# Kernel optimization log

Measured on AMD Instinct MI355X. Metric: run time of the kernel, lower is better.

## Reference

```python
import jax, jax.numpy as jnp
import numpy as np

B, C_IN, H, W = 4, 3, 512, 512
KH = KW = 3
K = KH * KW
C_OUT = 3
HO, WO = H - 2, W - 2  # valid conv, stride 1, no padding


def setup_inputs() -> dict:
    key = jax.random.key(0)
    k1, k2, k3, k4, k5, k6 = jax.random.split(key, 6)
    x = jax.random.normal(k1, (B, C_IN, H, W), dtype=jnp.float32)
    # conv1: Conv2d(3, 18, 3) -> predicts offsets (2*kh*kw = 18 channels)
    w1 = jax.random.normal(k2, (18, C_IN, KH, KW), dtype=jnp.float32) * 0.05
    b1 = jax.random.normal(k3, (18,), dtype=jnp.float32) * 0.05
    # conv2: DeformConv2d(3, 3, 3) weight + bias
    w2 = jax.random.normal(k4, (C_OUT, C_IN, KH, KW), dtype=jnp.float32) * 0.1
    b2 = jax.random.normal(k5, (C_OUT,), dtype=jnp.float32) * 0.1
    return {"x": x, "w1": w1, "b1": b1, "w2": w2, "b2": b2}


def _bilinear_gather(img, y, x):
    # img: [B, C, H, W]; y, x: [B, K, Ho, Wo] float sampling coords.
    # Bilinear interpolation with zeros outside the image (torchvision semantics).
    y0 = jnp.floor(y)
    x0 = jnp.floor(x)
    dy = y - y0
    dx = x - x0
    out = jnp.zeros((img.shape[0], img.shape[1]) + y.shape[1:], dtype=img.dtype)
    for iy, wy in ((y0, 1.0 - dy), (y0 + 1.0, dy)):
        for ix, wx in ((x0, 1.0 - dx), (x0 + 1.0, dx)):
            valid = (iy >= 0) & (iy < H) & (ix >= 0) & (ix < W)
            yi = jnp.clip(iy, 0, H - 1).astype(jnp.int32)
            xi = jnp.clip(ix, 0, W - 1).astype(jnp.int32)
            w = jnp.where(valid, wy * wx, 0.0)  # [B,K,Ho,Wo]
            g = jax.vmap(lambda im, a, b: im[:, a, b])(img, yi, xi)  # [B,C,K,Ho,Wo]
            out = out + g * w[:, None]
    return out


def _forward(x, w1, b1, w2, b2):
    dn = ("NCHW", "OIHW", "NCHW")
    # offset-predicting conv: [B, 18, Ho, Wo]
    offs = jax.lax.conv_general_dilated(x, w1, (1, 1), "VALID", dimension_numbers=dn)
    offs = offs + b1[None, :, None, None]
    # torchvision layout: channel 2k = dy, 2k+1 = dx for kernel tap k (row-major)
    off = offs.reshape(B, K, 2, HO, WO)
    ky = jnp.repeat(jnp.arange(KH, dtype=jnp.float32), KW)  # [K]
    kx = jnp.tile(jnp.arange(KW, dtype=jnp.float32), KH)    # [K]
    gy = jnp.arange(HO, dtype=jnp.float32)[None, None, :, None]
    gx = jnp.arange(WO, dtype=jnp.float32)[None, None, None, :]
    sy = gy + ky[None, :, None, None] + off[:, :, 0]  # [B,K,Ho,Wo]
    sx = gx + kx[None, :, None, None] + off[:, :, 1]
    val = _bilinear_gather(x, sy, sx)  # [B,C,K,Ho,Wo]
    w2r = w2.reshape(C_OUT, C_IN, K)
    out = jnp.einsum("ock,bckij->boij", w2r, val) + b2[None, :, None, None]
    return out


def reference(x, w1, b1, w2, b2):
    return _forward(x, w1, b1, w2, b2)
```

## Files before the change

### kernel.cpp

```cpp
#include <hip/hip_runtime.h>

#define BB 4
#define CIN 3
#define HH 512
#define WW 512
#define KK 9
#define COUT 3
#define HO 510
#define WO 510
#define HW (HH * WW)
#define HOWO (HO * WO)

#define PR 518
#define PC 520
#define PADR 3
#define PADC 4
#define XP_BYTES ((size_t)BB * PR * PC * sizeof(uint2))

typedef __fp16 h2 __attribute__((ext_vector_type(2)));

__device__ __forceinline__ h2 pkrtz(float a, float b) {
    return __builtin_amdgcn_cvt_pkrtz(a, b);
}
__device__ __forceinline__ float fdot2f(h2 a, h2 b, float c) {
    return __builtin_amdgcn_fdot2(a, b, c, false);
}
__device__ __forceinline__ h2 uint_as_h2(unsigned u) {
    return __builtin_bit_cast(h2, u);
}
__device__ __forceinline__ unsigned h2_as_uint(h2 h) {
    return __builtin_bit_cast(unsigned, h);
}
__device__ __forceinline__ float w1e(const float* w1, int ch, int c, int r, int s) {
    return w1[ch * 27 + c * 9 + r * 3 + s];
}

__global__ __launch_bounds__(256) void repack_padh(
    const float* __restrict__ x, uint2* __restrict__ xp)
{
    const int idx = blockIdx.x * blockDim.x + threadIdx.x;
    const int total = BB * PR * PC;
    if (idx >= total) return;
    const int b = idx / (PR * PC);
    const int rem = idx - b * (PR * PC);
    const int y = rem / PC;
    const int xc = rem - y * PC;
    const int ys = y - PADR;
    const int xs = xc - PADC;
    uint2 v = make_uint2(0u, 0u);
    if ((unsigned)ys < (unsigned)HH && (unsigned)xs < (unsigned)WW) {
        const float* xb = x + (size_t)b * CIN * HW;
        const int p = ys * WW + xs;
        v.x = h2_as_uint(pkrtz(xb[p], xb[HW + p]));
        v.y = h2_as_uint(pkrtz(xb[2 * HW + p], 0.f));
    }
    xp[idx] = v;
}

__global__ __launch_bounds__(256) void deform_fused5(
    const uint2* __restrict__ xp,
    const float* __restrict__ w1,
    const float* __restrict__ b1,
    const float* __restrict__ w2,
    const float* __restrict__ b2,
    float* __restrict__ out)
{
    __shared__ uint4 s_w1h[KK * 9];
    __shared__ float s_b[18];
    __shared__ float s_w2[KK * 12];
    __shared__ float s_b2[COUT];

    if (threadIdx.x < KK * 9) {
        const int k = threadIdx.x / 9;
        const int pos = threadIdx.x % 9;
        const int r = pos / 3, s = pos % 3;
        uint4 u;
        u.x = h2_as_uint(pkrtz(w1e(w1, 2 * k, 0, r, s), w1e(w1, 2 * k, 1, r, s)));
        u.y = h2_as_uint(pkrtz(w1e(w1, 2 * k, 2, r, s), 0.f));
        u.z = h2_as_uint(pkrtz(w1e(w1, 2 * k + 1, 0, r, s), w1e(w1, 2 * k + 1, 1, r, s)));
        u.w = h2_as_uint(pkrtz(w1e(w1, 2 * k + 1, 2, r, s), 0.f));
        s_w1h[threadIdx.x] = u;
    }
    for (int t = threadIdx.x; t < KK * 12; t += 256) {
        const int k = t / 12;
        const int q = t % 12;
        s_w2[t] = (q < 9) ? w2[(q / 3) * 27 + (q % 3) * 9 + k] : 0.f;
    }
    if (threadIdx.x < 18) s_b[threadIdx.x] = b1[threadIdx.x];
    if (threadIdx.x < COUT) s_b2[threadIdx.x] = b2[threadIdx.x];
    __syncthreads();

    constexpr int WP = WO / 2;
    const int idx = blockIdx.x * 256 + threadIdx.x;
    if (idx >= BB * HO * WP) return;
    const int jp = idx % WP;
    const int t1 = idx / WP;
    const int i = t1 % HO;
    const int b = t1 / HO;
    const int j = jp * 2;

    const uint2* xb2 = xp + (size_t)b * (PR * PC);

    h2 p01[3][4], p2p[3][4];
#pragma unroll
    for (int r = 0; r < 3; ++r) {
        const int base = (i + r + PADR) * PC + (j + PADC);
        const uint4 qa = *reinterpret_cast<const uint4*>(xb2 + base);
        const uint4 qb = *reinterpret_cast<const uint4*>(xb2 + base + 2);
        p01[r][0] = uint_as_h2(qa.x); p2p[r][0] = uint_as_h2(qa.y);
        p01[r][1] = uint_as_h2(qa.z); p2p[r][1] = uint_as_h2(qa.w);
        p01[r][2] = uint_as_h2(qb.x); p2p[r][2] = uint_as_h2(qb.y);
        p01[r][3] = uint_as_h2(qb.z); p2p[r][3] = uint_as_h2(qb.w);
    }

    unsigned pk0[KK], pk1[KK];
#pragma unroll
    for (int k = 0; k < KK; ++k) {
        float dy0 = s_b[2 * k], dx0 = s_b[2 * k + 1];
        float dy1 = dy0, dx1 = dx0;
        const uint4* wk = &s_w1h[k * 9];
#pragma unroll
        for (int r = 0; r < 3; ++r)
#pragma unroll
            for (int s = 0; s < 3; ++s) {
                const uint4 wq = wk[r * 3 + s];
                const h2 wy01 = uint_as_h2(wq.x);
                const h2 wy2x = uint_as_h2(wq.y);
                const h2 wx01 = uint_as_h2(wq.z);
                const h2 wx2x = uint_as_h2(wq.w);
                dy0 = fdot2f(wy01, p01[r][s], dy0);
                dy0 = fdot2f(wy2x, p2p[r][s], dy0);
                dx0 = fdot2f(wx01, p01[r][s], dx0);
                dx0 = fdot2f(wx2x, p2p[r][s], dx0);
                dy1 = fdot2f(wy01, p01[r][s + 1], dy1);
                dy1 = fdot2f(wy2x, p2p[r][s + 1], dy1);
                dx1 = fdot2f(wx01, p01[r][s + 1], dx1);
                dx1 = fdot2f(wx2x, p2p[r][s + 1], dx1);
            }
        pk0[k] = h2_as_uint(pkrtz(dy0, dx0));
        pk1[k] = h2_as_uint(pkrtz(dy1, dx1));
    }

    const float fi = (float)(i + PADR);
    const float fj = (float)(j + PADC);
    float acc00 = s_b2[0], acc01 = s_b2[1], acc02 = s_b2[2];
    float acc10 = s_b2[0], acc11 = s_b2[1], acc12 = s_b2[2];

#pragma unroll
    for (int k = 0; k < KK; ++k) {
        const float4* wk4 = reinterpret_cast<const float4*>(&s_w2[k * 12]);
        const float4 a = wk4[0];
        const float4 bbv = wk4[1];
        const float cw = s_w2[k * 12 + 8];
        const float ry = fi + (float)(k / 3);
        const float rx = fj + (float)(k % 3);

#pragma unroll
        for (int p = 0; p < 2; ++p) {
            const h2 d = uint_as_h2(p ? pk1[k] : pk0[k]);
            const float syp = ry + (float)d.x;
            const float sxp = rx + (float)p + (float)d.y;
            const int y0 = (int)syp;
            const int x0 = (int)sxp;
            const float fy = syp - (float)y0;
            const float fx = sxp - (float)x0;

            const int a00 = y0 * PC + x0;
            const uint2 c00 = xb2[a00];
            const uint2 c01 = xb2[a00 + 1];
            const uint2 c10 = xb2[a00 + PC];
            const uint2 c11 = xb2[a00 + PC + 1];

            const float wy0 = 1.f - fy, wx0 = 1.f - fx;
            const float w00 = wy0 * wx0, w01 = wy0 * fx;
            const float w10 = fy * wx0, w11 = fy * fx;

            const h2 g00 = uint_as_h2(c00.x), e00 = uint_as_h2(c00.y);
            const h2 g01 = uint_as_h2(c01.x), e01 = uint_as_h2(c01.y);
            const h2 g10 = uint_as_h2(c10.x), e10 = uint_as_h2(c10.y);
            const h2 g11 = uint_as_h2(c11.x), e11 = uint_as_h2(c11.y);

            const float v0 = w00 * (float)g00.x + w01 * (float)g01.x +
                             w10 * (float)g10.x + w11 * (float)g11.x;
            const float v1 = w00 * (float)g00.y + w01 * (float)g01.y +
                             w10 * (float)g10.y + w11 * (float)g11.y;
            const float v2 = w00 * (float)e00.x + w01 * (float)e01.x +
                             w10 * (float)e10.x + w11 * (float)e11.x;

            const float r0 = a.x * v0 + a.y * v1 + a.z * v2;
            const float r1 = a.w * v0 + bbv.x * v1 + bbv.y * v2;
            const float r2 = bbv.z * v0 + bbv.w * v1 + cw * v2;
            if (p == 0) {
                acc00 += r0; acc01 += r1; acc02 += r2;
            } else {
                acc10 += r0; acc11 += r1; acc12 += r2;
            }
        }
    }

    float* ob = out + (size_t)b * COUT * HOWO + (size_t)i * WO + j;
    {
        float2 st;
        st.x = acc00; st.y = acc10;
        *reinterpret_cast<float2*>(&ob[0 * HOWO]) = st;
        st.x = acc01; st.y = acc11;
        *reinterpret_cast<float2*>(&ob[1 * HOWO]) = st;
        st.x = acc02; st.y = acc12;
        *reinterpret_cast<float2*>(&ob[2 * HOWO]) = st;
    }
}

__global__ __launch_bounds__(256) void deform_fused_kernel(
    const float* __restrict__ x, const float* __restrict__ w1,
    const float* __restrict__ b1, const float* __restrict__ w2,
    const float* __restrict__ b2, float* __restrict__ out)
{
    __shared__ float s_w1[18 * 27];
    __shared__ float s_b1[18];
    __shared__ float s_w2[COUT * CIN * KK];
    __shared__ float s_b2[COUT];
    for (int t = threadIdx.x; t < 18 * 27; t += blockDim.x) s_w1[t] = w1[t];
    if (threadIdx.x < 18) s_b1[threadIdx.x] = b1[threadIdx.x];
    if (threadIdx.x < COUT * CIN * KK) s_w2[threadIdx.x] = w2[threadIdx.x];
    if (threadIdx.x < COUT) s_b2[threadIdx.x] = b2[threadIdx.x];
    __syncthreads();
    const int idx = blockIdx.x * blockDim.x + threadIdx.x;
    if (idx >= BB * HOWO) return;
    const int j = idx % WO;
    const int tmp = idx / WO;
    const int i = tmp % HO;
    const int b = tmp / HO;
    const float* xb = x + (size_t)b * CIN * HW;
    float patch[CIN][3][3];
#pragma unroll
    for (int c = 0; c < CIN; ++c)
#pragma unroll
        for (int r = 0; r < 3; ++r)
#pragma unroll
            for (int s = 0; s < 3; ++s)
                patch[c][r][s] = xb[c * HW + (i + r) * WW + (j + s)];
    float acc0 = s_b2[0], acc1 = s_b2[1], acc2 = s_b2[2];
#pragma unroll
    for (int k = 0; k < KK; ++k) {
        const int ky = k / 3, kx = k % 3;
        float dy = s_b1[2 * k], dx = s_b1[2 * k + 1];
        const float* wy = &s_w1[(2 * k) * 27];
        const float* wx = &s_w1[(2 * k + 1) * 27];
        int t = 0;
#pragma unroll
        for (int c = 0; c < CIN; ++c)
#pragma unroll
            for (int r = 0; r < 3; ++r)
#pragma unroll
                for (int s = 0; s < 3; ++s, ++t) {
                    const float pv = patch[c][r][s];
                    dy += pv * wy[t];
                    dx += pv * wx[t];
                }
        const float sy = (float)(i + ky) + dy;
        const float sx = (float)(j + kx) + dx;
        const float y0f = floorf(sy), x0f = floorf(sx);
        const float fy = sy - y0f, fx = sx - x0f;
        const int y0 = (int)y0f, x0 = (int)x0f;
        float v0 = 0.f, v1 = 0.f, v2 = 0.f;
#pragma unroll
        for (int cy = 0; cy < 2; ++cy) {
            const int iy = y0 + cy;
            const float wyf = cy ? fy : (1.f - fy);
            const bool vy = (iy >= 0) && (iy < HH);
            const int iyc = iy < 0 ? 0 : (iy > HH - 1 ? HH - 1 : iy);
#pragma unroll
            for (int cx = 0; cx < 2; ++cx) {
                const int ix = x0 + cx;
                const float wxf = cx ? fx : (1.f - fx);
                const bool vx = (ix >= 0) && (ix < WW);
                const int ixc = ix < 0 ? 0 : (ix > WW - 1 ? WW - 1 : ix);
                const float wgt = (vy && vx) ? (wyf * wxf) : 0.f;
                const int off = iyc * WW + ixc;
                v0 += wgt * xb[0 * HW + off];
                v1 += wgt * xb[1 * HW + off];
                v2 += wgt * xb[2 * HW + off];
            }
        }
#pragma unroll
        for (int o = 0; o < COUT; ++o) {
            const float c0 = s_w2[(o * CIN + 0) * KK + k];
            const float c1 = s_w2[(o * CIN + 1) * KK + k];
            const float c2 = s_w2[(o * CIN + 2) * KK + k];
            const float contrib = c0 * v0 + c1 * v1 + c2 * v2;
            if (o == 0) acc0 += contrib;
            else if (o == 1) acc1 += contrib;
            else acc2 += contrib;
        }
    }
    float* ob = out + (size_t)b * COUT * HOWO + (size_t)i * WO + j;
    ob[0 * HOWO] = acc0;
    ob[1 * HOWO] = acc1;
    ob[2 * HOWO] = acc2;
}

extern "C" void kernel_launch(void* const* d_in, const int* in_sizes, int n_in,
                              void* d_out, int out_size, void* d_ws, size_t ws_size,
                              hipStream_t stream) {
    const float* x  = (const float*)d_in[0];
    const float* w1 = (const float*)d_in[1];
    const float* b1 = (const float*)d_in[2];
    const float* w2 = (const float*)d_in[3];
    const float* b2 = (const float*)d_in[4];
    float* out = (float*)d_out;

    if (ws_size >= XP_BYTES) {
        uint2* xp = (uint2*)d_ws;
        {
            const int total = BB * PR * PC;
            repack_padh<<<(total + 255) / 256, 256, 0, stream>>>(x, xp);
        }
        {
            const int total = BB * HO * (WO / 2);
            deform_fused5<<<(total + 255) / 256, 256, 0, stream>>>(
                xp, w1, b1, w2, b2, out);
        }
    } else {
        const int total = BB * HOWO;
        deform_fused_kernel<<<(total + 255) / 256, 256, 0, stream>>>(
            x, w1, b1, w2, b2, out);
    }
}
```

Baseline: 44.08 us.

## Pack horizontal pixel pairs in the repacked image and do bilinear blending in packed fp16

The repack kernel now stores each padded pixel together with its right neighbour as one 16-byte fp16 record. Each bilinear tap then needs two vector loads (top and bottom rows) instead of four 8-byte loads. The interpolation is done with packed half multiply-adds, and the output-channel mix uses fdot2 with fp16-packed w2 weights, which cuts scalar FMA and conversion work. The trade-offs are a workspace twice as large, roughly double the repack write traffic, and lower precision from accumulating the interpolation in fp16.

```diff
diff --git a/kernel.cpp b/kernel.cpp
--- a/kernel.cpp
+++ b/kernel.cpp
@@ -15,7 +15,7 @@
 #define PC 520
 #define PADR 3
 #define PADC 4
-#define XP_BYTES ((size_t)BB * PR * PC * sizeof(uint2))
+#define XP_BYTES ((size_t)BB * PR * PC * sizeof(uint4))
 
 typedef __fp16 h2 __attribute__((ext_vector_type(2)));
 
@@ -35,8 +35,8 @@
     return w1[ch * 27 + c * 9 + r * 3 + s];
 }
 
-__global__ __launch_bounds__(256) void repack_padh(
-    const float* __restrict__ x, uint2* __restrict__ xp)
+__global__ __launch_bounds__(256) void repack_pairh(
+    const float* __restrict__ x, uint4* __restrict__ xp)
 {
     const int idx = blockIdx.x * blockDim.x + threadIdx.x;
     const int total = BB * PR * PC;
@@ -46,19 +46,28 @@
     const int y = rem / PC;
     const int xc = rem - y * PC;
     const int ys = y - PADR;
-    const int xs = xc - PADC;
-    uint2 v = make_uint2(0u, 0u);
-    if ((unsigned)ys < (unsigned)HH && (unsigned)xs < (unsigned)WW) {
-        const float* xb = x + (size_t)b * CIN * HW;
-        const int p = ys * WW + xs;
-        v.x = h2_as_uint(pkrtz(xb[p], xb[HW + p]));
-        v.y = h2_as_uint(pkrtz(xb[2 * HW + p], 0.f));
-    }
+    const float* xb = x + (size_t)b * CIN * HW;
+    float c[2][3] = {{0.f, 0.f, 0.f}, {0.f, 0.f, 0.f}};
+#pragma unroll
+    for (int q = 0; q < 2; ++q) {
+        const int xs = xc - PADC + q;
+        if ((unsigned)ys < (unsigned)HH && (unsigned)xs < (unsigned)WW) {
+            const int p = ys * WW + xs;
+            c[q][0] = xb[p];
+            c[q][1] = xb[HW + p];
+            c[q][2] = xb[2 * HW + p];
+        }
+    }
+    uint4 v;
+    v.x = h2_as_uint(pkrtz(c[0][0], c[0][1]));
+    v.y = h2_as_uint(pkrtz(c[0][2], 0.f));
+    v.z = h2_as_uint(pkrtz(c[1][0], c[1][1]));
+    v.w = h2_as_uint(pkrtz(c[1][2], 0.f));
     xp[idx] = v;
 }
 
-__global__ __launch_bounds__(256) void deform_fused5(
-    const uint2* __restrict__ xp,
+__global__ __launch_bounds__(256) void deform_fused6(
+    const uint4* __restrict__ xp,
     const float* __restrict__ w1,
     const float* __restrict__ b1,
     const float* __restrict__ w2,
@@ -67,7 +76,8 @@
 {
     __shared__ uint4 s_w1h[KK * 9];
     __shared__ float s_b[18];
-    __shared__ float s_w2[KK * 12];
+    __shared__ uint4 s_w2a[KK];
+    __shared__ uint2 s_w2b[KK];
     __shared__ float s_b2[COUT];
 
     if (threadIdx.x < KK * 9) {
@@ -81,10 +91,18 @@
         u.w = h2_as_uint(pkrtz(w1e(w1, 2 * k + 1, 2, r, s), 0.f));
         s_w1h[threadIdx.x] = u;
     }
-    for (int t = threadIdx.x; t < KK * 12; t += 256) {
-        const int k = t / 12;
-        const int q = t % 12;
-        s_w2[t] = (q < 9) ? w2[(q / 3) * 27 + (q % 3) * 9 + k] : 0.f;
+    if (threadIdx.x < KK) {
+        const int k = threadIdx.x;
+        uint4 wa;
+        wa.x = h2_as_uint(pkrtz(w2[k], w2[9 + k]));
+        wa.y = h2_as_uint(pkrtz(w2[18 + k], 0.f));
+        wa.z = h2_as_uint(pkrtz(w2[27 + k], w2[36 + k]));
+        wa.w = h2_as_uint(pkrtz(w2[45 + k], 0.f));
+        s_w2a[k] = wa;
+        uint2 wb;
+        wb.x = h2_as_uint(pkrtz(w2[54 + k], w2[63 + k]));
+        wb.y = h2_as_uint(pkrtz(w2[72 + k], 0.f));
+        s_w2b[k] = wb;
     }
     if (threadIdx.x < 18) s_b[threadIdx.x] = b1[threadIdx.x];
     if (threadIdx.x < COUT) s_b2[threadIdx.x] = b2[threadIdx.x];
@@ -99,14 +117,14 @@
     const int b = t1 / HO;
     const int j = jp * 2;
 
-    const uint2* xb2 = xp + (size_t)b * (PR * PC);
+    const uint4* xb4 = xp + (size_t)b * (PR * PC);
 
     h2 p01[3][4], p2p[3][4];
 #pragma unroll
     for (int r = 0; r < 3; ++r) {
         const int base = (i + r + PADR) * PC + (j + PADC);
-        const uint4 qa = *reinterpret_cast<const uint4*>(xb2 + base);
-        const uint4 qb = *reinterpret_cast<const uint4*>(xb2 + base + 2);
+        const uint4 qa = xb4[base];
+        const uint4 qb = xb4[base + 2];
         p01[r][0] = uint_as_h2(qa.x); p2p[r][0] = uint_as_h2(qa.y);
         p01[r][1] = uint_as_h2(qa.z); p2p[r][1] = uint_as_h2(qa.w);
         p01[r][2] = uint_as_h2(qb.x); p2p[r][2] = uint_as_h2(qb.y);
@@ -148,10 +166,8 @@
 
 #pragma unroll
     for (int k = 0; k < KK; ++k) {
-        const float4* wk4 = reinterpret_cast<const float4*>(&s_w2[k * 12]);
-        const float4 a = wk4[0];
-        const float4 bbv = wk4[1];
-        const float cw = s_w2[k * 12 + 8];
+        const uint4 wa = s_w2a[k];
+        const uint2 wb = s_w2b[k];
         const float ry = fi + (float)(k / 3);
         const float rx = fj + (float)(k % 3);
 
@@ -166,34 +182,39 @@
             const float fx = sxp - (float)x0;
 
             const int a00 = y0 * PC + x0;
-            const uint2 c00 = xb2[a00];
-            const uint2 c01 = xb2[a00 + 1];
-            const uint2 c10 = xb2[a00 + PC];
-            const uint2 c11 = xb2[a00 + PC + 1];
+            const uint4 top = xb4[a00];
+            const uint4 bot = xb4[a00 + PC];
 
             const float wy0 = 1.f - fy, wx0 = 1.f - fx;
             const float w00 = wy0 * wx0, w01 = wy0 * fx;
             const float w10 = fy * wx0, w11 = fy * fx;
-
-            const h2 g00 = uint_as_h2(c00.x), e00 = uint_as_h2(c00.y);
-            const h2 g01 = uint_as_h2(c01.x), e01 = uint_as_h2(c01.y);
-            const h2 g10 = uint_as_h2(c10.x), e10 = uint_as_h2(c10.y);
-            const h2 g11 = uint_as_h2(c11.x), e11 = uint_as_h2(c11.y);
-
-            const float v0 = w00 * (float)g00.x + w01 * (float)g01.x +
-                             w10 * (float)g10.x + w11 * (float)g11.x;
-            const float v1 = w00 * (float)g00.y + w01 * (float)g01.y +
-                             w10 * (float)g10.y + w11 * (float)g11.y;
-            const float v2 = w00 * (float)e00.x + w01 * (float)e01.x +
-                             w10 * (float)e10.x + w11 * (float)e11.x;
-
-            const float r0 = a.x * v0 + a.y * v1 + a.z * v2;
-            const float r1 = a.w * v0 + bbv.x * v1 + bbv.y * v2;
-            const float r2 = bbv.z * v0 + bbv.w * v1 + cw * v2;
+            const h2 h00 = pkrtz(w00, w00);
+            const h2 h01 = pkrtz(w01, w01);
+            const h2 h10 = pkrtz(w10, w10);
+            const h2 h11 = pkrtz(w11, w11);
+
+            const h2 g00 = uint_as_h2(top.x), e00 = uint_as_h2(top.y);
+            const h2 g01 = uint_as_h2(top.z), e01 = uint_as_h2(top.w);
+            const h2 g10 = uint_as_h2(bot.x), e10 = uint_as_h2(bot.y);
+            const h2 g11 = uint_as_h2(bot.z), e11 = uint_as_h2(bot.w);
+
+            h2 vg = h00 * g00;
+            vg = h01 * g01 + vg;
+            vg = h10 * g10 + vg;
+            vg = h11 * g11 + vg;
+            h2 ve = h00 * e00;
+            ve = h01 * e01 + ve;
+            ve = h10 * e10 + ve;
+            ve = h11 * e11 + ve;
+
             if (p == 0) {
-                acc00 += r0; acc01 += r1; acc02 += r2;
+                acc00 = fdot2f(uint_as_h2(wa.x), vg, fdot2f(uint_as_h2(wa.y), ve, acc00));
+                acc01 = fdot2f(uint_as_h2(wa.z), vg, fdot2f(uint_as_h2(wa.w), ve, acc01));
+                acc02 = fdot2f(uint_as_h2(wb.x), vg, fdot2f(uint_as_h2(wb.y), ve, acc02));
             } else {
-                acc10 += r0; acc11 += r1; acc12 += r2;
+                acc10 = fdot2f(uint_as_h2(wa.x), vg, fdot2f(uint_as_h2(wa.y), ve, acc10));
+                acc11 = fdot2f(uint_as_h2(wa.z), vg, fdot2f(uint_as_h2(wa.w), ve, acc11));
+                acc12 = fdot2f(uint_as_h2(wb.x), vg, fdot2f(uint_as_h2(wb.y), ve, acc12));
             }
         }
     }
@@ -310,14 +331,14 @@
     float* out = (float*)d_out;
 
     if (ws_size >= XP_BYTES) {
-        uint2* xp = (uint2*)d_ws;
+        uint4* xp = (uint4*)d_ws;
         {
             const int total = BB * PR * PC;
-            repack_padh<<<(total + 255) / 256, 256, 0, stream>>>(x, xp);
+            repack_pairh<<<(total + 255) / 256, 256, 0, stream>>>(x, xp);
         }
         {
             const int total = BB * HO * (WO / 2);
-            deform_fused5<<<(total + 255) / 256, 256, 0, stream>>>(
+            deform_fused6<<<(total + 255) / 256, 256, 0, stream>>>(
                 xp, w1, b1, w2, b2, out);
         }
     } else {
```

Measured after the change: 48.97 us. +11.1%, slower.
